# Optimization experiments

Hardware: AMD Instinct MI355X
Metric: run time of the kernel (lower is better)

Reference implementation:

```python
import jax, jax.numpy as jnp
import numpy as np

N_FEAT = 64
N_PROJ = 32
N_OUT = 128
LN_EPS = 1e-5


def setup_inputs() -> dict:
    key = jax.random.key(0)
    ks = jax.random.split(key, 8)
    n_seq, n_res = 256, 384
    M = jax.random.normal(ks[0], (1, n_seq, n_res, N_FEAT), dtype=jnp.float32)
    M_mask = jnp.ones((1, n_seq, n_res), dtype=jnp.float32)
    Z_raw = jax.random.normal(ks[1], (1, n_res, n_res, N_OUT), dtype=jnp.float32)
    s = 1.0 / np.sqrt(N_FEAT)
    Wa = jax.random.uniform(ks[2], (N_PROJ, N_FEAT), jnp.float32, -s, s)
    ba = jnp.zeros((N_PROJ,), jnp.float32)
    Wb = jax.random.uniform(ks[3], (N_PROJ, N_FEAT), jnp.float32, -s, s)
    bb = jnp.zeros((N_PROJ,), jnp.float32)
    so = 1.0 / np.sqrt(N_PROJ * N_PROJ)
    Wo = jax.random.uniform(ks[4], (N_OUT, N_PROJ * N_PROJ), jnp.float32, -so, so)
    bo = jnp.zeros((N_OUT,), jnp.float32)
    gamma = jnp.ones((N_FEAT,), jnp.float32)
    beta = jnp.zeros((N_FEAT,), jnp.float32)
    return {"M": M, "M_mask": M_mask, "Z_raw": Z_raw, "gamma": gamma, "beta": beta,
            "Wa": Wa, "ba": ba, "Wb": Wb, "bb": bb, "Wo": Wo, "bo": bo}


def reference(M, M_mask, Z_raw, gamma, beta, Wa, ba, Wb, bb, Wo, bo):
    # LayerNorm over last dim
    mu = jnp.mean(M, axis=-1, keepdims=True)
    var = jnp.mean(jnp.square(M - mu), axis=-1, keepdims=True)
    Mn = (M - mu) * jax.lax.rsqrt(var + LN_EPS) * gamma + beta
    # projections [1, s, r, p]
    left = jnp.einsum('bsrf,pf->bsrp', Mn, Wa) + ba
    right = jnp.einsum('bsrf,pf->bsrp', Mn, Wb) + bb
    mask = M_mask[..., None]  # [1, s, r, 1]
    left = mask * left
    right = mask * right
    # norm[i,j] = sum_s mask[s,i]*mask[s,j]
    norm = jnp.einsum('sa,sd->ad', M_mask[0], M_mask[0])[None, :, :, None]
    n_res, p = left.shape[2], left.shape[3]
    # outer-product mean: O[i,j,c,d] = sum_s left[s,i,c] * right[s,j,d]
    O = jnp.einsum('sic,sjd->ijcd', left[0], right[0])
    O = O.reshape(n_res, n_res, p * p)
    Z = jnp.einsum('ijk,ok->ijo', O, Wo) + bo  # [r, r, n_out]
    Z = Z[None] / (0.001 + norm)
    return Z + Z_raw
```

## Files before the change

### kernel.cpp

```cpp
#include <hip/hip_runtime.h>

typedef unsigned short u16;
typedef u16   u16x4 __attribute__((ext_vector_type(4)));
typedef u16   u16x8 __attribute__((ext_vector_type(8)));
typedef short s16x8 __attribute__((ext_vector_type(8)));
typedef float f32x4 __attribute__((ext_vector_type(4)));

#define NSEQ 256
#define NRES 384
#define NF   64
#define NP   32
#define NO   128

__device__ __forceinline__ u16 f2b(float f) {
    union { float f; unsigned u; } c; c.f = f;
    unsigned r = c.u + 0x7fffu + ((c.u >> 16) & 1u);
    return (u16)(r >> 16);
}

__device__ __forceinline__ void gload_lds16(const u16* g, u16* l) {
    __builtin_amdgcn_global_load_lds(
        (const __attribute__((address_space(1))) unsigned int*)(g),
        (__attribute__((address_space(3))) unsigned int*)(l),
        16, 0, 0);
}

__global__ __launch_bounds__(256) void k_pre(
    const float* __restrict__ M, const float* __restrict__ mask,
    const float* __restrict__ gamma, const float* __restrict__ beta,
    const float* __restrict__ Wa, const float* __restrict__ ba,
    const float* __restrict__ Wb, const float* __restrict__ bb,
    const float* __restrict__ Wo,
    u16* __restrict__ leftT, u16* __restrict__ rightT,
    float* __restrict__ normMat, u16* __restrict__ WoB)
{
    __shared__ __align__(16) char sm[34816];
    const int b = blockIdx.x, t = threadIdx.x;

    if (b < 1536) {
        float (*Mt)[68] = (float (*)[68])sm;
        float* gs   = (float*)(sm + 17408);
        float* bs   = gs + 64;
        float* bias = bs + 64;
        float* mk   = bias + 64;
        const int i  = b % NRES;
        const int s0 = (b / NRES) * 64;
        const int s  = t >> 2, f0 = (t & 3) * 16;

        {
            const float* g = M + ((long)(s0 + s) * NRES + i) * NF + f0;
            #pragma unroll
            for (int q = 0; q < 4; ++q) {
                f32x4 v = *(const f32x4*)(g + q * 4);
                #pragma unroll
                for (int e = 0; e < 4; ++e) Mt[s][f0 + q * 4 + e] = v[e];
            }
        }
        if (t < 64) { gs[t] = gamma[t]; bs[t] = beta[t];
                      mk[t] = mask[(long)(s0 + t) * NRES + i]; }
        if (t < 32) { bias[t] = ba[t]; bias[32 + t] = bb[t]; }
        __syncthreads();

        float sum = 0.f, sq = 0.f;
        #pragma unroll
        for (int e = 0; e < 16; ++e) { float v = Mt[s][f0 + e]; sum += v; sq += v * v; }
        sum += __shfl_xor(sum, 1); sq += __shfl_xor(sq, 1);
        sum += __shfl_xor(sum, 2); sq += __shfl_xor(sq, 2);
        float mu  = sum * (1.f / 64.f);
        float var = sq * (1.f / 64.f) - mu * mu;
        float rs  = rsqrtf(var + 1e-5f);
        #pragma unroll
        for (int e = 0; e < 16; ++e) {
            int f = f0 + e;
            Mt[s][f] = (Mt[s][f] - mu) * rs * gs[f] + bs[f];
        }
        __syncthreads();

        const int sg = t >> 6, rowid = t & 63;
        const int lr = rowid >> 5, p = rowid & 31;
        const float* Wg = (lr ? Wb : Wa) + p * 64;
        f32x4 wreg[16];
        #pragma unroll
        for (int q = 0; q < 16; ++q) wreg[q] = *(const f32x4*)(Wg + q * 4);

        float accv[16];
        #pragma unroll
        for (int e = 0; e < 16; ++e) accv[e] = 0.f;
        #pragma unroll 4
        for (int f4 = 0; f4 < 16; ++f4) {
            f32x4 w4 = wreg[f4];
            #pragma unroll
            for (int e = 0; e < 16; ++e) {
                f32x4 m4 = *(const f32x4*)(&Mt[sg * 16 + e][f4 * 4]);
                accv[e] += m4[0]*w4[0] + m4[1]*w4[1] + m4[2]*w4[2] + m4[3]*w4[3];
            }
        }
        const float b_ = bias[rowid];
        u16x8 o0, o1;
        #pragma unroll
        for (int e = 0; e < 8; ++e) o0[e] = f2b((accv[e]     + b_) * mk[sg * 16 + e]);
        #pragma unroll
        for (int e = 0; e < 8; ++e) o1[e] = f2b((accv[8 + e] + b_) * mk[sg * 16 + 8 + e]);
        u16* dst = (lr ? rightT : leftT) + ((long)i * NP + p) * NSEQ + s0 + sg * 16;
        *(u16x8*)dst       = o0;
        *(u16x8*)(dst + 8) = o1;

    } else if (b < 1664) {
        int idx = (b - 1536) * 256 + t;
        int o   = idx >> 8;
        int kp  = (idx & 255) << 2;
        int l16 = (kp >> 2) & 15;
        int ntb = (kp >> 6) & 1;
        int qd  = (kp >> 7) & 3;
        int mtb = (kp >> 9) & 1;
        const float* src = Wo + o * 1024 + (mtb * 16 + qd * 4) * 32 + ntb * 16 + l16;
        u16x4 w;
        #pragma unroll
        for (int rg = 0; rg < 4; ++rg) w[rg] = f2b(src[rg * 32]);
        *(u16x4*)(WoB + o * 1024 + kp) = w;

    } else {
        float (*mi)[17] = (float (*)[17])sm;
        float (*mj)[17] = (float (*)[17])(sm + 17408);
        const int bn = b - 1664;
        const int iB = (bn / 24) * 16, jB = (bn % 24) * 16;
        #pragma unroll
        for (int it = 0; it < 16; ++it) {
            int ss = it * 16 + (t >> 4);
            int c  = t & 15;
            mi[ss][c] = mask[(long)ss * NRES + iB + c];
            mj[ss][c] = mask[(long)ss * NRES + jB + c];
        }
        __syncthreads();
        const int ti = t >> 4, tj = t & 15;
        float acc = 0.f;
        for (int ss = 0; ss < 256; ++ss) acc += mi[ss][ti] * mj[ss][tj];
        normMat[(long)(iB + ti) * NRES + jB + tj] = acc;
    }
}

__global__ __launch_bounds__(512, 4) void k_main(
    const u16* __restrict__ leftT, const u16* __restrict__ rightT,
    const float* __restrict__ normMat,
    const u16* __restrict__ WoB, const float* __restrict__ bo,
    const float* __restrict__ Zraw, float* __restrict__ out)
{
    __shared__ __align__(16) u16 smem[32768];

    const int t    = threadIdx.x;
    const int wave = t >> 6, lane = t & 63;
    const int quad = lane >> 4, l16 = lane & 15;
    const int wr = wave >> 1, wc = wave & 1;

    const int bid = blockIdx.x;
    const int r_  = bid >> 3;
    const int bx  = r_ / 12;
    const int by  = (bid & 7) * 12 + (r_ % 12);
    const int icBase = bx * 256;
    const int jdBase = by * 128;

    const int srow = lane >> 2;
    const int g8   = ((lane & 3) ^ ((srow >> 1) & 3)) * 8;

    f32x4 acc[4][4] = {};

    const u16* aSrc0 = leftT  + (icBase + wave * 32 + srow) * NSEQ + g8;
    const u16* aSrc1 = aSrc0 + 16 * NSEQ;
    const u16* bSrc  = rightT + (jdBase + wave * 16 + srow) * NSEQ + g8;

    #define STAGE(buf, k0) do {                                                  \
        gload_lds16(aSrc0 + (k0), &smem[(buf) * 8192 + wave * 1024]);            \
        gload_lds16(aSrc1 + (k0), &smem[(buf) * 8192 + wave * 1024 + 512]);      \
        gload_lds16(bSrc  + (k0), &smem[16384 + (buf) * 4096 + wave * 512]);     \
    } while (0)

    STAGE(0, 0);

    #pragma unroll
    for (int kt = 0; kt < 8; ++kt) {
        const int cur = kt & 1;
        if (kt < 7) {
            STAGE(cur ^ 1, (kt + 1) * 32);
            asm volatile("s_waitcnt vmcnt(3)" ::: "memory");
        } else {
            asm volatile("s_waitcnt vmcnt(0)" ::: "memory");
        }
        __builtin_amdgcn_s_barrier();
        __builtin_amdgcn_sched_barrier(0);

        const int gx = (quad ^ ((l16 >> 1) & 3)) * 8;
        u16x8 af[4], bf[4];
        const u16* Ab = &smem[cur * 8192 + (wr * 64 + l16) * 32 + gx];
        const u16* Bb = &smem[16384 + cur * 4096 + (wc * 64 + l16) * 32 + gx];
        #pragma unroll
        for (int mt = 0; mt < 4; ++mt) af[mt] = *(const u16x8*)(Ab + mt * 512);
        #pragma unroll
        for (int nt = 0; nt < 4; ++nt) bf[nt] = *(const u16x8*)(Bb + nt * 512);

        #pragma unroll
        for (int mt = 0; mt < 4; ++mt)
            #pragma unroll
            for (int nt = 0; nt < 4; ++nt)
                acc[mt][nt] = __builtin_amdgcn_mfma_f32_16x16x32_bf16(
                    (s16x8)af[mt], (s16x8)bf[nt], acc[mt][nt], 0, 0, 0);

        __builtin_amdgcn_sched_barrier(0);
        __builtin_amdgcn_s_barrier();
    }
    #undef STAGE

    #pragma unroll
    for (int mt = 0; mt < 4; ++mt) {
        #pragma unroll
        for (int nt = 0; nt < 4; ++nt) {
            int pair = (wr * 2 + (mt >> 1)) * 4 + wc * 2 + (nt >> 1);
            int kp   = l16 * 4 + (nt & 1) * 64 + quad * 128 + (mt & 1) * 512;
            int ks   = kp ^ (quad << 4) ^ ((pair & 7) << 3);
            u16x4 wv;
            #pragma unroll
            for (int rg = 0; rg < 4; ++rg) wv[rg] = f2b(acc[mt][nt][rg]);
            *(u16x4*)&smem[pair * 1024 + ks] = wv;
        }
    }
    __syncthreads();

    f32x4 acc2[2] = {};
    const int ob   = wave * 16;
    const int pxor = (l16 & 7) << 3;
    const u16* wp  = WoB + (ob + l16) * 1024 + quad * 8;
    const u16* os0 = &smem[l16 * 1024];
    const u16* os1 = &smem[(16 + l16) * 1024];
    #pragma unroll 4
    for (int kk = 0; kk < 32; ++kk) {
        int kp = kk * 32 + quad * 8;
        int ks = kp ^ (((kp >> 7) & 3) << 4) ^ pxor;
        u16x8 a0 = *(const u16x8*)(os0 + ks);
        u16x8 a1 = *(const u16x8*)(os1 + ks);
        u16x8 bv = *(const u16x8*)(wp + kk * 32);
        acc2[0] = __builtin_amdgcn_mfma_f32_16x16x32_bf16((s16x8)a0, (s16x8)bv, acc2[0], 0, 0, 0);
        acc2[1] = __builtin_amdgcn_mfma_f32_16x16x32_bf16((s16x8)a1, (s16x8)bv, acc2[1], 0, 0, 0);
    }
    __syncthreads();

    float* zs = (float*)smem;
    #pragma unroll
    for (int m = 0; m < 2; ++m)
        #pragma unroll
        for (int rg = 0; rg < 4; ++rg)
            zs[(m * 16 + quad * 4 + rg) * 128 + ob + l16] = acc2[m][rg];
    __syncthreads();

    const int i0 = bx * 8, j0 = by * 4;
    const int pr = t >> 4, o0 = (t & 15) * 8;
    const int i = i0 + (pr >> 2), j = j0 + (pr & 3);
    const float rn = 1.f / (0.001f + normMat[i * NRES + j]);
    const long base = ((long)(i * NRES + j)) * NO + o0;
    f32x4 z0  = *(const f32x4*)&zs[pr * 128 + o0];
    f32x4 z1  = *(const f32x4*)&zs[pr * 128 + o0 + 4];
    f32x4 zr0 = *(const f32x4*)(Zraw + base);
    f32x4 zr1 = *(const f32x4*)(Zraw + base + 4);
    f32x4 bv0 = *(const f32x4*)(bo + o0);
    f32x4 bv1 = *(const f32x4*)(bo + o0 + 4);
    f32x4 r0, r1;
    #pragma unroll
    for (int e = 0; e < 4; ++e) r0[e] = (z0[e] + bv0[e]) * rn + zr0[e];
    #pragma unroll
    for (int e = 0; e < 4; ++e) r1[e] = (z1[e] + bv1[e]) * rn + zr1[e];
    *(f32x4*)(out + base)     = r0;
    *(f32x4*)(out + base + 4) = r1;
}

extern "C" void kernel_launch(void* const* d_in, const int* in_sizes, int n_in,
                              void* d_out, int out_size, void* d_ws, size_t ws_size,
                              hipStream_t stream)
{
    const float* M     = (const float*)d_in[0];
    const float* mask  = (const float*)d_in[1];
    const float* Zraw  = (const float*)d_in[2];
    const float* gamma = (const float*)d_in[3];
    const float* beta  = (const float*)d_in[4];
    const float* Wa    = (const float*)d_in[5];
    const float* ba    = (const float*)d_in[6];
    const float* Wb    = (const float*)d_in[7];
    const float* bb    = (const float*)d_in[8];
    const float* Wo    = (const float*)d_in[9];
    const float* bo    = (const float*)d_in[10];
    float* out = (float*)d_out;

    char* ws = (char*)d_ws;
    u16*   leftT   = (u16*)ws;
    u16*   rightT  = (u16*)(ws + 6291456);
    float* normMat = (float*)(ws + 12582912);
    u16*   WoB     = (u16*)(ws + 13172736);

    k_pre<<<dim3(2240), dim3(256), 0, stream>>>(M, mask, gamma, beta,
                                                Wa, ba, Wb, bb, Wo,
                                                leftT, rightT, normMat, WoB);
    k_main<<<dim3(4608), dim3(512), 0, stream>>>(leftT, rightT, normMat,
                                                 WoB, bo, Zraw, out);
}
```

Before: 387.5 us.

## Move LayerNorm projection to split-bf16 MFMA and add setprio around MFMA loops

The projection in k_pre, previously done with scalar FP32 FMAs, now runs on MFMA. Normalized activations and weights are each split into hi/lo bf16 parts and combined with three MFMAs per tile, which keeps close to FP32 accuracy. M is loaded straight into LDS with global_load_lds using swizzled layouts, and each block covers a 16-residue by 8-sequence tile, so the grid shrinks from 2240 to 1472 blocks. k_main also wraps its MFMA sections in s_setprio and unrolls the second GEMM loop further. The risks are the smaller per-store write granularity (4 bf16 values per store) and the extra LDS use, which may lower occupancy.

Measured after the change: 341.8 us. 11.8% less time.

```diff
diff --git a/kernel.cpp b/kernel.cpp
--- a/kernel.cpp
+++ b/kernel.cpp
@@ -16,6 +16,10 @@
     union { float f; unsigned u; } c; c.f = f;
     unsigned r = c.u + 0x7fffu + ((c.u >> 16) & 1u);
     return (u16)(r >> 16);
+}
+__device__ __forceinline__ float b2f(u16 h) {
+    union { unsigned u; float f; } c; c.u = ((unsigned)h) << 16;
+    return c.f;
 }
 
 __device__ __forceinline__ void gload_lds16(const u16* g, u16* l) {
@@ -34,79 +38,158 @@
     u16* __restrict__ leftT, u16* __restrict__ rightT,
     float* __restrict__ normMat, u16* __restrict__ WoB)
 {
-    __shared__ __align__(16) char sm[34816];
+    __shared__ __align__(16) char sm[52480];
     const int b = blockIdx.x, t = threadIdx.x;
 
-    if (b < 1536) {
-        float (*Mt)[68] = (float (*)[68])sm;
-        float* gs   = (float*)(sm + 17408);
-        float* bs   = gs + 64;
-        float* bias = bs + 64;
-        float* mk   = bias + 64;
-        const int i  = b % NRES;
-        const int s0 = (b / NRES) * 64;
-        const int s  = t >> 2, f0 = (t & 3) * 16;
+    if (b < 768) {
+        const int sC = b / 24, iC = b % 24;
+        const int i0 = iC * 16, s0 = sC * 8;
+
+        u16*   hiP   = (u16*)sm;
+        u16*   loP   = (u16*)sm + 8192;
+        u16*   WP    = (u16*)(sm + 32768);
+        float* mkP   = (float*)(sm + 51200);
+        float* biasP = (float*)(sm + 51712);
+        float* glP   = (float*)(sm + 51968);
+        float* blP   = (float*)(sm + 52224);
+
+        const int wv = t >> 6, ln = t & 63;
+        const int quad = ln >> 4, l16 = ln & 15;
 
         {
-            const float* g = M + ((long)(s0 + s) * NRES + i) * NF + f0;
-            #pragma unroll
-            for (int q = 0; q < 4; ++q) {
-                f32x4 v = *(const f32x4*)(g + q * 4);
+            const int rl = ln >> 4, c = ln & 15;
+            #pragma unroll
+            for (int q = 0; q < 8; ++q) {
+                int rbase = wv * 32 + q * 4;
+                int r   = rbase + rl;
+                int xsw = (r & 3) << 1;
+                const float* src = M + ((long)(s0 + (r & 7)) * NRES + (i0 + (r >> 3))) * NF
+                                     + ((c ^ xsw) << 2);
+                gload_lds16((const u16*)src, (u16*)sm + rbase * 128);
+            }
+        }
+        {
+            const int side = t >> 7, p = (t >> 2) & 31, qq = t & 3;
+            const float* Wg = (side ? Wb : Wa) + p * 64 + qq * 16;
+            u16x8 h[2], l[2];
+            #pragma unroll
+            for (int u = 0; u < 4; ++u) {
+                f32x4 w4 = *(const f32x4*)(Wg + u * 4);
                 #pragma unroll
-                for (int e = 0; e < 4; ++e) Mt[s][f0 + q * 4 + e] = v[e];
-            }
-        }
-        if (t < 64) { gs[t] = gamma[t]; bs[t] = beta[t];
-                      mk[t] = mask[(long)(s0 + t) * NRES + i]; }
-        if (t < 32) { bias[t] = ba[t]; bias[32 + t] = bb[t]; }
+                for (int e = 0; e < 4; ++e) {
+                    u16 hb = f2b(w4[e]);
+                    h[u >> 1][(u & 1) * 4 + e] = hb;
+                    l[u >> 1][(u & 1) * 4 + e] = f2b(w4[e] - b2f(hb));
+                }
+            }
+            int hbase = ((side * 2 + 0) * 32 + p) * 72 + qq * 16;
+            int lbase = ((side * 2 + 1) * 32 + p) * 72 + qq * 16;
+            *(u16x8*)(WP + hbase)     = h[0];
+            *(u16x8*)(WP + hbase + 8) = h[1];
+            *(u16x8*)(WP + lbase)     = l[0];
+            *(u16x8*)(WP + lbase + 8) = l[1];
+        }
+        if (t < 128) mkP[t] = mask[(long)(s0 + (t & 7)) * NRES + i0 + (t >> 3)];
+        if (t < 64) { glP[t] = gamma[t]; blP[t] = beta[t];
+                      biasP[t] = (t < 32) ? ba[t] : bb[t - 32]; }
         __syncthreads();
 
+        const int r = t >> 1, half = t & 1;
+        const int xsw = (r & 3) << 1, psw = r & 3;
+        f32x4 v[8];
+        {
+            const float* raw = (const float*)sm + r * 64;
+            #pragma unroll
+            for (int e = 0; e < 8; ++e)
+                v[e] = *(const f32x4*)(raw + (((half * 8 + e) ^ xsw) << 2));
+        }
         float sum = 0.f, sq = 0.f;
         #pragma unroll
-        for (int e = 0; e < 16; ++e) { float v = Mt[s][f0 + e]; sum += v; sq += v * v; }
+        for (int e = 0; e < 8; ++e)
+            #pragma unroll
+            for (int j = 0; j < 4; ++j) { float x = v[e][j]; sum += x; sq += x * x; }
         sum += __shfl_xor(sum, 1); sq += __shfl_xor(sq, 1);
-        sum += __shfl_xor(sum, 2); sq += __shfl_xor(sq, 2);
         float mu  = sum * (1.f / 64.f);
         float var = sq * (1.f / 64.f) - mu * mu;
         float rs  = rsqrtf(var + 1e-5f);
         #pragma unroll
-        for (int e = 0; e < 16; ++e) {
-            int f = f0 + e;
-            Mt[s][f] = (Mt[s][f] - mu) * rs * gs[f] + bs[f];
+        for (int e = 0; e < 8; ++e) {
+            int og = half * 8 + e;
+            f32x4 g4 = *(const f32x4*)(glP + og * 4);
+            f32x4 b4 = *(const f32x4*)(blP + og * 4);
+            #pragma unroll
+            for (int j = 0; j < 4; ++j) v[e][j] = (v[e][j] - mu) * rs * g4[j] + b4[j];
         }
         __syncthreads();
 
-        const int sg = t >> 6, rowid = t & 63;
-        const int lr = rowid >> 5, p = rowid & 31;
-        const float* Wg = (lr ? Wb : Wa) + p * 64;
-        f32x4 wreg[16];
-        #pragma unroll
-        for (int q = 0; q < 16; ++q) wreg[q] = *(const f32x4*)(Wg + q * 4);
-
-        float accv[16];
-        #pragma unroll
-        for (int e = 0; e < 16; ++e) accv[e] = 0.f;
-        #pragma unroll 4
-        for (int f4 = 0; f4 < 16; ++f4) {
-            f32x4 w4 = wreg[f4];
-            #pragma unroll
-            for (int e = 0; e < 16; ++e) {
-                f32x4 m4 = *(const f32x4*)(&Mt[sg * 16 + e][f4 * 4]);
-                accv[e] += m4[0]*w4[0] + m4[1]*w4[1] + m4[2]*w4[2] + m4[3]*w4[3];
-            }
-        }
-        const float b_ = bias[rowid];
-        u16x8 o0, o1;
-        #pragma unroll
-        for (int e = 0; e < 8; ++e) o0[e] = f2b((accv[e]     + b_) * mk[sg * 16 + e]);
-        #pragma unroll
-        for (int e = 0; e < 8; ++e) o1[e] = f2b((accv[8 + e] + b_) * mk[sg * 16 + 8 + e]);
-        u16* dst = (lr ? rightT : leftT) + ((long)i * NP + p) * NSEQ + s0 + sg * 16;
-        *(u16x8*)dst       = o0;
-        *(u16x8*)(dst + 8) = o1;
-
-    } else if (b < 1664) {
-        int idx = (b - 1536) * 256 + t;
+        #pragma unroll
+        for (int d = 0; d < 4; ++d) {
+            u16x8 h8, l8;
+            #pragma unroll
+            for (int j = 0; j < 4; ++j) {
+                u16 hb = f2b(v[2 * d][j]);
+                h8[j] = hb; l8[j] = f2b(v[2 * d][j] - b2f(hb));
+                u16 hb2 = f2b(v[2 * d + 1][j]);
+                h8[4 + j] = hb2; l8[4 + j] = f2b(v[2 * d + 1][j] - b2f(hb2));
+            }
+            int q = (half * 4 + d) ^ psw;
+            *(u16x8*)(hiP + r * 64 + q * 8) = h8;
+            *(u16x8*)(loP + r * 64 + q * 8) = l8;
+        }
+        __syncthreads();
+
+        const int wbase = wv * 32;
+        f32x4 acc[2][4] = {};
+        #pragma unroll
+        for (int k = 0; k < 2; ++k) {
+            u16x8 ah[2], al[2];
+            #pragma unroll
+            for (int rt = 0; rt < 2; ++rt) {
+                int row = wbase + rt * 16 + l16;
+                int gk  = (quad + k * 4) ^ (row & 3);
+                ah[rt] = *(const u16x8*)(hiP + row * 64 + gk * 8);
+                al[rt] = *(const u16x8*)(loP + row * 64 + gk * 8);
+            }
+            #pragma unroll
+            for (int pt = 0; pt < 4; ++pt) {
+                int side = pt >> 1, ph = pt & 1;
+                int hrow = ((side * 2 + 0) * 32 + ph * 16 + l16) * 72 + (quad + k * 4) * 8;
+                int lrow = ((side * 2 + 1) * 32 + ph * 16 + l16) * 72 + (quad + k * 4) * 8;
+                u16x8 bh = *(const u16x8*)(WP + hrow);
+                u16x8 bl = *(const u16x8*)(WP + lrow);
+                #pragma unroll
+                for (int rt = 0; rt < 2; ++rt) {
+                    acc[rt][pt] = __builtin_amdgcn_mfma_f32_16x16x32_bf16(
+                        (s16x8)ah[rt], (s16x8)bh, acc[rt][pt], 0, 0, 0);
+                    acc[rt][pt] = __builtin_amdgcn_mfma_f32_16x16x32_bf16(
+                        (s16x8)al[rt], (s16x8)bh, acc[rt][pt], 0, 0, 0);
+                    acc[rt][pt] = __builtin_amdgcn_mfma_f32_16x16x32_bf16(
+                        (s16x8)ah[rt], (s16x8)bl, acc[rt][pt], 0, 0, 0);
+                }
+            }
+        }
+
+        #pragma unroll
+        for (int rt = 0; rt < 2; ++rt) {
+            int rowb = wbase + rt * 16 + quad * 4;
+            f32x4 mk4 = *(const f32x4*)(mkP + rowb);
+            int ii = rowb >> 3, sb = rowb & 7;
+            #pragma unroll
+            for (int pt = 0; pt < 4; ++pt) {
+                int side = pt >> 1, p = (pt & 1) * 16 + l16;
+                float bv = biasP[side * 32 + p];
+                u16x4 ov;
+                #pragma unroll
+                for (int rg = 0; rg < 4; ++rg)
+                    ov[rg] = f2b((acc[rt][pt][rg] + bv) * mk4[rg]);
+                u16* dst = (side ? rightT : leftT)
+                         + ((long)(i0 + ii) * NP + p) * NSEQ + s0 + sb;
+                *(u16x4*)dst = ov;
+            }
+        }
+
+    } else if (b < 896) {
+        int idx = (b - 768) * 256 + t;
         int o   = idx >> 8;
         int kp  = (idx & 255) << 2;
         int l16 = (kp >> 2) & 15;
@@ -122,7 +205,7 @@
     } else {
         float (*mi)[17] = (float (*)[17])sm;
         float (*mj)[17] = (float (*)[17])(sm + 17408);
-        const int bn = b - 1664;
+        const int bn = b - 896;
         const int iB = (bn / 24) * 16, jB = (bn % 24) * 16;
         #pragma unroll
         for (int it = 0; it < 16; ++it) {
@@ -197,12 +280,14 @@
         #pragma unroll
         for (int nt = 0; nt < 4; ++nt) bf[nt] = *(const u16x8*)(Bb + nt * 512);
 
+        __builtin_amdgcn_s_setprio(1);
         #pragma unroll
         for (int mt = 0; mt < 4; ++mt)
             #pragma unroll
             for (int nt = 0; nt < 4; ++nt)
                 acc[mt][nt] = __builtin_amdgcn_mfma_f32_16x16x32_bf16(
                     (s16x8)af[mt], (s16x8)bf[nt], acc[mt][nt], 0, 0, 0);
+        __builtin_amdgcn_s_setprio(0);
 
         __builtin_amdgcn_sched_barrier(0);
         __builtin_amdgcn_s_barrier();
@@ -230,15 +315,17 @@
     const u16* wp  = WoB + (ob + l16) * 1024 + quad * 8;
     const u16* os0 = &smem[l16 * 1024];
     const u16* os1 = &smem[(16 + l16) * 1024];
-    #pragma unroll 4
+    #pragma unroll 8
     for (int kk = 0; kk < 32; ++kk) {
         int kp = kk * 32 + quad * 8;
         int ks = kp ^ (((kp >> 7) & 3) << 4) ^ pxor;
         u16x8 a0 = *(const u16x8*)(os0 + ks);
         u16x8 a1 = *(const u16x8*)(os1 + ks);
         u16x8 bv = *(const u16x8*)(wp + kk * 32);
+        __builtin_amdgcn_s_setprio(1);
         acc2[0] = __builtin_amdgcn_mfma_f32_16x16x32_bf16((s16x8)a0, (s16x8)bv, acc2[0], 0, 0, 0);
         acc2[1] = __builtin_amdgcn_mfma_f32_16x16x32_bf16((s16x8)a1, (s16x8)bv, acc2[1], 0, 0, 0);
+        __builtin_amdgcn_s_setprio(0);
     }
     __syncthreads();
 
@@ -293,7 +380,7 @@
     float* normMat = (float*)(ws + 12582912);
     u16*   WoB     = (u16*)(ws + 13172736);
 
-    k_pre<<<dim3(2240), dim3(256), 0, stream>>>(M, mask, gamma, beta,
+    k_pre<<<dim3(1472), dim3(256), 0, stream>>>(M, mask, gamma, beta,
                                                 Wa, ba, Wb, bb, Wo,
                                                 leftT, rightT, normMat, WoB);
     k_main<<<dim3(4608), dim3(512), 0, stream>>>(leftT, rightT, normMat,
```
